# Optimization experiments

Hardware: AMD Instinct MI355X
Metric: run time of the kernel (lower is better)

## Reference

```python
import jax, jax.numpy as jnp
import numpy as np

N = 50000      # nodes
E = 800000     # edges (avg degree 16)
INDIM = 128
OUTDIM = 64


def setup_inputs() -> dict:
    key = jax.random.key(0)
    k1, k2, k3, k4, k5 = jax.random.split(key, 5)
    h = jax.random.normal(k1, (N, INDIM), dtype=jnp.float32)
    W = jax.random.normal(k2, (INDIM, OUTDIM), dtype=jnp.float32) * 0.05
    Wa = jax.random.normal(k3, (2 * OUTDIM,), dtype=jnp.float32) * 0.05
    src = jax.random.randint(k4, (E,), 0, N)
    dst = jax.random.randint(k5, (E,), 0, N)
    return {"h": h, "W": W, "Wa": Wa, "src": src, "dst": dst}


def reference(h, W, Wa, src, dst):
    # node transform: n_mlp_layer=1, bias=False MultiLinearLayer == one linear
    z = h @ W  # [N, OUTDIM]
    # edge attention: relu(attn_linear(cat(z_src, z_dst)))
    # avoid materializing [E, 2*OUTDIM] concat: split Wa into src/dst halves
    s = z @ Wa[:OUTDIM]   # [N] src contribution
    t = z @ Wa[OUTDIM:]   # [N] dst contribution
    e = jax.nn.relu(s[src] + t[dst])  # [E]
    # segment softmax over incoming edges of each destination node
    m = jax.ops.segment_max(e, dst, num_segments=N)      # [N]
    ex = jnp.exp(e - m[dst])                             # [E]
    denom = jax.ops.segment_sum(ex, dst, num_segments=N) # [N]
    alpha = ex / denom[dst]                              # [E]
    # weighted scatter-sum aggregation of src features (dropout p=0 -> identity)
    h_out = jax.ops.segment_sum(alpha[:, None] * z[src], dst, num_segments=N)
    # batch_norm=False; final activation relu; dropout p=0 -> identity
    return jax.nn.relu(h_out)
```

## Files before the change

### kernel.cpp

```cpp
#include <hip/hip_runtime.h>
#include <math.h>

#define INDIM 128
#define OUTDIM 64
#define HK 136
#define CP 68
#define SCHUNK 2048

typedef __bf16 bf16x8 __attribute__((ext_vector_type(8)));
typedef float f32x4 __attribute__((ext_vector_type(4)));
typedef unsigned short ushortx8 __attribute__((ext_vector_type(8)));

static __device__ __forceinline__ unsigned short f2bf(float f) {
    unsigned u = __float_as_uint(f);
    u += 0x7FFFu + ((u >> 16) & 1u);
    return (unsigned short)(u >> 16);
}
static __device__ __forceinline__ float bf2f(unsigned short b) {
    return __uint_as_float((unsigned)b << 16);
}

__global__ __launch_bounds__(256) void nt_count(
    const float* __restrict__ h, const float* __restrict__ W,
    const float* __restrict__ Wa, unsigned short* __restrict__ z,
    float* __restrict__ s, float* __restrict__ t,
    const int* __restrict__ dst, int* __restrict__ bcnt,
    int N, int E, int gemm_blocks)
{
    __shared__ __align__(16) unsigned short smem[2 * 64 * HK];
    unsigned short* As = smem;
    unsigned short* Bs = smem + 64 * HK;
    float* Cs = (float*)smem;
    int tid = threadIdx.x;

    if (blockIdx.x >= gemm_blocks) {
        int* l = (int*)smem;
        l[tid] = 0;
        __syncthreads();
        int base = (blockIdx.x - gemm_blocks) * 8192;
        #pragma unroll 2
        for (int u = 0; u < 8; ++u) {
            int i = base + (u * 256 + tid) * 4;
            if (i + 3 < E) {
                int4 d4 = *(const int4*)&dst[i];
                atomicAdd(&l[d4.x >> 8], 1);
                atomicAdd(&l[d4.y >> 8], 1);
                atomicAdd(&l[d4.z >> 8], 1);
                atomicAdd(&l[d4.w >> 8], 1);
            } else {
                for (int q = i; q < E; ++q) atomicAdd(&l[dst[q] >> 8], 1);
            }
        }
        __syncthreads();
        if (l[tid]) atomicAdd(bcnt + tid, l[tid]);
        return;
    }

    int node0 = blockIdx.x * 64;
    int nv = min(64, N - node0);

    {
        const float4* hg = (const float4*)(h + (size_t)node0 * INDIM);
        #pragma unroll
        for (int i = 0; i < 8; ++i) {
            int idx = i * 256 + tid;
            int n = idx >> 5, j = idx & 31;
            float4 v = (n < nv) ? hg[n * 32 + j] : make_float4(0.f, 0.f, 0.f, 0.f);
            ushort4 b = make_ushort4(f2bf(v.x), f2bf(v.y), f2bf(v.z), f2bf(v.w));
            *(ushort4*)&As[n * HK + j * 4] = b;
        }
    }
    {
        const float4* Wg = (const float4*)W;
        #pragma unroll
        for (int u = 0; u < 8; ++u) {
            int idx = u * 256 + tid;
            int k = idx >> 4;
            int n0 = (idx & 15) * 4;
            float4 v = Wg[idx];
            Bs[(n0 + 0) * HK + k] = f2bf(v.x);
            Bs[(n0 + 1) * HK + k] = f2bf(v.y);
            Bs[(n0 + 2) * HK + k] = f2bf(v.z);
            Bs[(n0 + 3) * HK + k] = f2bf(v.w);
        }
    }
    __syncthreads();

    int wv = tid >> 6, l = tid & 63;
    int lr = l & 15, lg = l >> 4;

    f32x4 acc[4];
    #pragma unroll
    for (int nf = 0; nf < 4; ++nf) acc[nf] = (f32x4){0.f, 0.f, 0.f, 0.f};

    #pragma unroll
    for (int ks = 0; ks < 4; ++ks) {
        int k0 = ks * 32 + lg * 8;
        bf16x8 a = *(const bf16x8*)&As[(wv * 16 + lr) * HK + k0];
        #pragma unroll
        for (int nf = 0; nf < 4; ++nf) {
            bf16x8 b = *(const bf16x8*)&Bs[(nf * 16 + lr) * HK + k0];
            acc[nf] = __builtin_amdgcn_mfma_f32_16x16x32_bf16(a, b, acc[nf], 0, 0, 0);
        }
    }

    __syncthreads();

    #pragma unroll
    for (int nf = 0; nf < 4; ++nf)
        #pragma unroll
        for (int r = 0; r < 4; ++r)
            Cs[(wv * 16 + lg * 4 + r) * CP + nf * 16 + lr] = acc[nf][r];

    int row = wv * 16 + (l >> 2);
    int cq = l & 3;
    int node = node0 + row;
    float ssum = 0.f, tsum = 0.f;
    #pragma unroll
    for (int qq = 0; qq < 2; ++qq) {
        int c0 = cq * 16 + qq * 8;
        float4 ca = *(const float4*)&Cs[row * CP + c0];
        float4 cb = *(const float4*)&Cs[row * CP + c0 + 4];
        float4 wsa = *(const float4*)&Wa[c0];
        float4 wsb = *(const float4*)&Wa[c0 + 4];
        float4 wta = *(const float4*)&Wa[OUTDIM + c0];
        float4 wtb = *(const float4*)&Wa[OUTDIM + c0 + 4];
        ssum += ca.x * wsa.x + ca.y * wsa.y + ca.z * wsa.z + ca.w * wsa.w
              + cb.x * wsb.x + cb.y * wsb.y + cb.z * wsb.z + cb.w * wsb.w;
        tsum += ca.x * wta.x + ca.y * wta.y + ca.z * wta.z + ca.w * wta.w
              + cb.x * wtb.x + cb.y * wtb.y + cb.z * wtb.z + cb.w * wtb.w;
        if (node < N) {
            ushortx8 zb;
            zb[0] = f2bf(ca.x); zb[1] = f2bf(ca.y);
            zb[2] = f2bf(ca.z); zb[3] = f2bf(ca.w);
            zb[4] = f2bf(cb.x); zb[5] = f2bf(cb.y);
            zb[6] = f2bf(cb.z); zb[7] = f2bf(cb.w);
            *(ushortx8*)&z[(size_t)node * OUTDIM + c0] = zb;
        }
    }
    ssum += __shfl_xor(ssum, 1, 64);
    ssum += __shfl_xor(ssum, 2, 64);
    tsum += __shfl_xor(tsum, 1, 64);
    tsum += __shfl_xor(tsum, 2, 64);
    if (cq == 0 && node < N) {
        s[node] = ssum;
        t[node] = tsum;
    }
}

__global__ __launch_bounds__(256) void bucket_scatter(
    const int* __restrict__ src, const int* __restrict__ dst,
    const int* __restrict__ bcnt, int* __restrict__ gcursor,
    int* __restrict__ esort, int E)
{
    __shared__ int lcnt[256];
    __shared__ int loff[256];
    __shared__ int gbase[256];
    __shared__ int lcur[256];
    __shared__ int bs[256];
    __shared__ int stage[SCHUNK];
    __shared__ unsigned char bof[SCHUNK];
    int tid = threadIdx.x;
    int base = blockIdx.x * SCHUNK;
    int ne = min(SCHUNK, E - base);

    int bc = bcnt[tid];
    bs[tid] = bc;
    lcnt[tid] = 0;
    __syncthreads();
    for (int off = 1; off < 256; off <<= 1) {
        int add = (tid >= off) ? bs[tid - off] : 0;
        __syncthreads();
        bs[tid] += add;
        __syncthreads();
    }
    int bstart_own = bs[tid] - bc;

    int mys[8], myd[8];
    #pragma unroll
    for (int u = 0; u < 8; ++u) {
        int li = u * 256 + tid;
        if (li < ne) {
            mys[u] = src[base + li];
            myd[u] = dst[base + li];
            atomicAdd(&lcnt[myd[u] >> 8], 1);
        } else myd[u] = -1;
    }
    __syncthreads();

    loff[tid] = lcnt[tid];
    __syncthreads();
    for (int off = 1; off < 256; off <<= 1) {
        int add = (tid >= off) ? loff[tid - off] : 0;
        __syncthreads();
        loff[tid] += add;
        __syncthreads();
    }
    int excl = loff[tid] - lcnt[tid];
    loff[tid] = excl;
    lcur[tid] = excl;
    if (lcnt[tid] > 0)
        gbase[tid] = bstart_own + atomicAdd(gcursor + tid, lcnt[tid]);
    __syncthreads();

    #pragma unroll
    for (int u = 0; u < 8; ++u) {
        if (myd[u] >= 0) {
            int b = myd[u] >> 8;
            int p = atomicAdd(&lcur[b], 1);
            stage[p] = ((myd[u] & 255) << 24) | mys[u];
            bof[p] = (unsigned char)b;
        }
    }
    __syncthreads();

    for (int i = tid; i < ne; i += 256) {
        int b = bof[i];
        esort[gbase[b] + (i - loff[b])] = stage[i];
    }
}

__global__ __launch_bounds__(256) void bucket_fill(
    const int* __restrict__ esort, const int* __restrict__ bcnt,
    int* __restrict__ counts, int* __restrict__ offsets,
    int* __restrict__ srcs, int N)
{
    __shared__ int bs[256];
    __shared__ int cnt[256];
    __shared__ int off[256];
    __shared__ int cur[256];
    int tid = threadIdx.x;
    int b = blockIdx.x;

    int bc = bcnt[tid];
    bs[tid] = bc;
    cnt[tid] = 0;
    __syncthreads();
    for (int o = 1; o < 256; o <<= 1) {
        int add = (tid >= o) ? bs[tid - o] : 0;
        __syncthreads();
        bs[tid] += add;
        __syncthreads();
    }
    int e0 = (b > 0) ? bs[b - 1] : 0;
    int e1 = bs[b];
    int node0 = b << 8;

    for (int i = e0 + tid; i < e1; i += 256)
        atomicAdd(&cnt[((unsigned)esort[i]) >> 24], 1);
    __syncthreads();

    off[tid] = cnt[tid];
    __syncthreads();
    for (int o = 1; o < 256; o <<= 1) {
        int add = (tid >= o) ? off[tid - o] : 0;
        __syncthreads();
        off[tid] += add;
        __syncthreads();
    }
    int excl = off[tid] - cnt[tid];
    cur[tid] = excl;
    int node = node0 + tid;
    if (node < N) { counts[node] = cnt[tid]; offsets[node] = e0 + excl; }
    __syncthreads();

    for (int i = e0 + tid; i < e1; i += 256) {
        int pe = esort[i];
        int p = atomicAdd(&cur[((unsigned)pe) >> 24], 1);
        srcs[e0 + p] = pe & 0xFFFFFF;
    }
}

__global__ __launch_bounds__(256) void aggregate(
    const unsigned short* __restrict__ z, const int* __restrict__ srcs,
    const float* __restrict__ s, const float* __restrict__ t,
    const int* __restrict__ offsets, const int* __restrict__ counts,
    float* __restrict__ out, int N)
{
    __shared__ int   ls[8][64];
    __shared__ float le[8][64];
    int hw = threadIdx.x >> 5;
    int lane = threadIdx.x & 31;
    int node = blockIdx.x * 8 + hw;
    if (node >= N) return;
    int start = offsets[node];
    int deg = counts[node];
    float2 acc = make_float2(0.f, 0.f);

    if (deg > 0) {
        float tn = t[node];
        float se = 0.f;
        for (int c0 = 0; c0 < deg; c0 += 64) {
            int cn = min(64, deg - c0);
            float pe = 0.f;
            if (lane < cn) {
                int sj = srcs[start + c0 + lane];
                float e = __expf(fmaxf(s[sj] + tn, 0.f));
                ls[hw][lane] = sj; le[hw][lane] = e; pe += e;
            }
            if (lane + 32 < cn) {
                int sj = srcs[start + c0 + lane + 32];
                float e = __expf(fmaxf(s[sj] + tn, 0.f));
                ls[hw][lane + 32] = sj; le[hw][lane + 32] = e; pe += e;
            }
            #pragma unroll
            for (int off = 16; off; off >>= 1) pe += __shfl_xor(pe, off, 32);
            se += pe;

            int j = 0;
            for (; j + 8 <= cn; j += 8) {
                int si[8]; float ei[8]; ushort2 ai[8];
                #pragma unroll
                for (int u = 0; u < 8; ++u) { si[u] = ls[hw][j + u]; ei[u] = le[hw][j + u]; }
                #pragma unroll
                for (int u = 0; u < 8; ++u)
                    ai[u] = *(const ushort2*)&z[(size_t)si[u] * OUTDIM + lane * 2];
                #pragma unroll
                for (int u = 0; u < 8; ++u) {
                    acc.x += ei[u] * bf2f(ai[u].x);
                    acc.y += ei[u] * bf2f(ai[u].y);
                }
            }
            for (; j < cn; ++j) {
                int sj = ls[hw][j]; float ej = le[hw][j];
                ushort2 a = *(const ushort2*)&z[(size_t)sj * OUTDIM + lane * 2];
                acc.x += ej * bf2f(a.x);
                acc.y += ej * bf2f(a.y);
            }
        }
        float inv = 1.f / se;
        acc.x = fmaxf(acc.x * inv, 0.f);
        acc.y = fmaxf(acc.y * inv, 0.f);
    }
    *(float2*)&out[(size_t)node * OUTDIM + lane * 2] = acc;
}

extern "C" void kernel_launch(void* const* d_in, const int* in_sizes, int n_in,
                              void* d_out, int out_size, void* d_ws, size_t ws_size,
                              hipStream_t stream) {
    const float* h  = (const float*)d_in[0];
    const float* W  = (const float*)d_in[1];
    const float* Wa = (const float*)d_in[2];
    const int* src  = (const int*)d_in[3];
    const int* dst  = (const int*)d_in[4];
    int N = in_sizes[0] / INDIM;
    int E = in_sizes[3];
    float* out = (float*)d_out;
    int nbuck = (N + 255) >> 8;

    char* ws = (char*)d_ws;
    unsigned short* z = (unsigned short*)ws;  ws += (size_t)N * OUTDIM * 2;
    float* s       = (float*)ws;  ws += (size_t)N * 4;
    float* t       = (float*)ws;  ws += (size_t)N * 4;
    int*   srcs    = (int*)ws;    ws += (size_t)E * 4;
    int*   counts  = (int*)ws;    ws += (size_t)N * 4;
    int*   offsets = (int*)ws;    ws += (size_t)N * 4;
    int*   esort   = (int*)ws;    ws += (size_t)E * 4;
    int*   bcnt    = (int*)ws;    ws += 256 * 4;
    int*   gcursor = (int*)ws;    ws += 256 * 4;

    int gemm_blocks = (N + 63) / 64;
    int count_blocks = (E + 8191) / 8192;

    hipMemsetAsync(bcnt, 0, 512 * sizeof(int), stream);

    nt_count<<<gemm_blocks + count_blocks, 256, 0, stream>>>(
        h, W, Wa, z, s, t, dst, bcnt, N, E, gemm_blocks);
    bucket_scatter<<<(E + SCHUNK - 1) / SCHUNK, 256, 0, stream>>>(
        src, dst, bcnt, gcursor, esort, E);
    bucket_fill<<<nbuck, 256, 0, stream>>>(esort, bcnt, counts, offsets, srcs, N);
    aggregate<<<(N + 7) / 8, 256, 0, stream>>>(z, srcs, s, t, offsets, counts, out, N);
}
```

Measured before the change: 137.9 us.

## Pre-convert W to swizzled bf16 once and load it via global_load_lds

A new prep kernel converts W to bf16 a single time, stores it in an XOR-swizzled layout in workspace, and zeroes the bucket counters, which replaces the memset. Each GEMM block then copies the prepared W straight into LDS with direct global-to-LDS loads, instead of converting fp32 W and doing scattered transposed LDS writes in all ~780 blocks. The count blocks are moved to the front of the grid so they are scheduled first. In exchange this adds an extra small kernel launch and depends on the swizzled LDS read addressing being correct.

Result: no change. 136.4 us (-1.1%).

```diff
diff --git a/kernel.cpp b/kernel.cpp
--- a/kernel.cpp
+++ b/kernel.cpp
@@ -20,24 +20,44 @@
     return __uint_as_float((unsigned)b << 16);
 }
 
+__global__ __launch_bounds__(256) void prep(
+    const float* __restrict__ W, unsigned short* __restrict__ W2,
+    int* __restrict__ bcnt)
+{
+    int tid = threadIdx.x;
+    if (blockIdx.x == 0) {
+        bcnt[tid] = 0;
+        bcnt[tid + 256] = 0;
+        return;
+    }
+    int e0 = (blockIdx.x - 1) * 512 + tid * 2;
+    #pragma unroll
+    for (int u = 0; u < 2; ++u) {
+        int e = e0 + u;
+        int k = e >> 6, n = e & 63;
+        unsigned swz = ((unsigned)(n * 256 + 2 * k)) ^ ((unsigned)((n & 7) << 4));
+        W2[swz >> 1] = f2bf(W[e]);
+    }
+}
+
 __global__ __launch_bounds__(256) void nt_count(
-    const float* __restrict__ h, const float* __restrict__ W,
+    const float* __restrict__ h, const unsigned short* __restrict__ W2,
     const float* __restrict__ Wa, unsigned short* __restrict__ z,
     float* __restrict__ s, float* __restrict__ t,
     const int* __restrict__ dst, int* __restrict__ bcnt,
-    int N, int E, int gemm_blocks)
-{
-    __shared__ __align__(16) unsigned short smem[2 * 64 * HK];
+    int N, int E, int count_blocks)
+{
+    __shared__ __align__(16) unsigned short smem[64 * HK + 64 * 128];
     unsigned short* As = smem;
     unsigned short* Bs = smem + 64 * HK;
     float* Cs = (float*)smem;
     int tid = threadIdx.x;
 
-    if (blockIdx.x >= gemm_blocks) {
+    if (blockIdx.x < count_blocks) {
         int* l = (int*)smem;
         l[tid] = 0;
         __syncthreads();
-        int base = (blockIdx.x - gemm_blocks) * 8192;
+        int base = blockIdx.x * 8192;
         #pragma unroll 2
         for (int u = 0; u < 8; ++u) {
             int i = base + (u * 256 + tid) * 4;
@@ -56,8 +76,9 @@
         return;
     }
 
-    int node0 = blockIdx.x * 64;
+    int node0 = (blockIdx.x - count_blocks) * 64;
     int nv = min(64, N - node0);
+    int wv = tid >> 6, l = tid & 63;
 
     {
         const float4* hg = (const float4*)(h + (size_t)node0 * INDIM);
@@ -71,22 +92,18 @@
         }
     }
     {
-        const float4* Wg = (const float4*)W;
+        const unsigned short* gsrc = W2 + wv * 2048;
+        unsigned short* lbase = Bs + wv * 2048;
         #pragma unroll
-        for (int u = 0; u < 8; ++u) {
-            int idx = u * 256 + tid;
-            int k = idx >> 4;
-            int n0 = (idx & 15) * 4;
-            float4 v = Wg[idx];
-            Bs[(n0 + 0) * HK + k] = f2bf(v.x);
-            Bs[(n0 + 1) * HK + k] = f2bf(v.y);
-            Bs[(n0 + 2) * HK + k] = f2bf(v.z);
-            Bs[(n0 + 3) * HK + k] = f2bf(v.w);
-        }
-    }
-    __syncthreads();
-
-    int wv = tid >> 6, l = tid & 63;
+        for (int c = 0; c < 4; ++c) {
+            __builtin_amdgcn_global_load_lds(
+                (const __attribute__((address_space(1))) unsigned int*)(gsrc + c * 512 + l * 8),
+                (__attribute__((address_space(3))) unsigned int*)(lbase + c * 512),
+                16, 0, 0);
+        }
+    }
+    __syncthreads();
+
     int lr = l & 15, lg = l >> 4;
 
     f32x4 acc[4];
@@ -99,7 +116,9 @@
         bf16x8 a = *(const bf16x8*)&As[(wv * 16 + lr) * HK + k0];
         #pragma unroll
         for (int nf = 0; nf < 4; ++nf) {
-            bf16x8 b = *(const bf16x8*)&Bs[(nf * 16 + lr) * HK + k0];
+            unsigned boff = ((unsigned)((nf * 16 + lr) * 256 + 2 * k0))
+                          ^ ((unsigned)((lr & 7) << 4));
+            bf16x8 b = *(const bf16x8*)((const char*)Bs + boff);
             acc[nf] = __builtin_amdgcn_mfma_f32_16x16x32_bf16(a, b, acc[nf], 0, 0, 0);
         }
     }
@@ -358,14 +377,15 @@
     int*   esort   = (int*)ws;    ws += (size_t)E * 4;
     int*   bcnt    = (int*)ws;    ws += 256 * 4;
     int*   gcursor = (int*)ws;    ws += 256 * 4;
+    unsigned short* W2 = (unsigned short*)ws; ws += INDIM * OUTDIM * 2;
 
     int gemm_blocks = (N + 63) / 64;
     int count_blocks = (E + 8191) / 8192;
 
-    hipMemsetAsync(bcnt, 0, 512 * sizeof(int), stream);
+    prep<<<17, 256, 0, stream>>>(W, W2, bcnt);
 
     nt_count<<<gemm_blocks + count_blocks, 256, 0, stream>>>(
-        h, W, Wa, z, s, t, dst, bcnt, N, E, gemm_blocks);
+        h, W2, Wa, z, s, t, dst, bcnt, N, E, count_blocks);
     bucket_scatter<<<(E + SCHUNK - 1) / SCHUNK, 256, 0, stream>>>(
         src, dst, bcnt, gcursor, esort, E);
     bucket_fill<<<nbuck, 256, 0, stream>>>(esort, bcnt, counts, offsets, srcs, N);
```
